# Optimization experiments

Hardware: AMD Instinct MI355X
Metric: run time of the kernel (lower is better)

The kernel has to match this reference:

```python
import jax, jax.numpy as jnp
import numpy as np

L, B, DW, DH, W, NG = 1024, 64, 300, 256, 2, 1
NEG = -1e25


def window_context(hx, w):
    """Concat of 2w+1 time-shifted copies of hx [L,B,D] -> [L,B,(2w+1)D].
    Order matches torch: shift-down by w..1, identity, shift-up by 1..w."""
    Lh = hx.shape[0]
    parts = []
    for i in range(w, -w - 1, -1):
        if i > 0:
            p = jnp.concatenate([jnp.zeros_like(hx[:i]), hx[:Lh - i]], axis=0)
        elif i < 0:
            k = -i
            p = jnp.concatenate([hx[k:], jnp.zeros_like(hx[:k])], axis=0)
        else:
            p = hx
        parts.append(p)
    return jnp.concatenate(parts, axis=2)


def setup_inputs() -> dict:
    key = jax.random.key(0)
    ks = jax.random.split(key, 11)
    E = (2 * W + 1) * DH
    std = 0.1  # reset_parameters('normal') uses N(0, 0.1)
    return {
        "src_seq": jax.random.normal(ks[0], (L, B, DW), jnp.float32),
        "h0": jax.random.normal(ks[1], (L + NG, B, DH), jnp.float32),
        "c0": jax.random.normal(ks[2], (L + NG, B, DH), jnp.float32),
        # word-gate params stacked over gates (i,l,r,f,s,o,u)
        "Ww": std * jax.random.normal(ks[3], (7, DH, E), jnp.float32),
        "Wu": std * jax.random.normal(ks[4], (7, DH, DW), jnp.float32),
        "Wv": std * jax.random.normal(ks[5], (7, DH, DH), jnp.float32),
        "Wb": std * jax.random.normal(ks[6], (7, DH), jnp.float32),
        # sentence-gate params stacked over gates (g,f,o)
        "Sw": std * jax.random.normal(ks[7], (3, DH, DH), jnp.float32),
        "Su": std * jax.random.normal(ks[8], (3, DH, DH), jnp.float32),
        "Sb": std * jax.random.normal(ks[9], (3, DH), jnp.float32),
        "src_len": jax.random.randint(ks[10], (B, 1), 1, L + 1, jnp.int32),
    }


def reference(src_seq, h0, c0, Ww, Wu, Wv, Wb, Sw, Su, Sb, src_len):
    # seq_mask[t, b] = True where t >= length[b]  -> [L, B, 1]
    seq_mask = (jnp.arange(L)[:, None] >= src_len[:, 0][None, :])[:, :, None]

    h_g1 = h0[L:]                                 # [1,B,DH] sentence node
    c_g1 = c0[L:]
    h_w1 = jnp.where(seq_mask, 0.0, h0[:L])       # [L,B,DH] word nodes
    c_w1 = jnp.where(seq_mask, 0.0, c0[:L])
    h_hat = h_w1.mean(axis=0)                     # [B,DH]
    hg = h_g1[0]                                  # [B,DH]

    # --- sentence node update (gate order g,f,o) ---
    fg = jax.nn.sigmoid(hg @ Sw[0].T + h_hat @ Su[0].T + Sb[0])[None]   # [1,B,DH]
    og = jax.nn.sigmoid(hg @ Sw[2].T + h_hat @ Su[2].T + Sb[2])[None]
    fi = jax.nn.sigmoid((hg @ Sw[1].T)[None]
                        + jnp.einsum('lbh,dh->lbd', h_w1, Su[1]) + Sb[1])
    fi = jnp.where(seq_mask, NEG, fi)
    fi_n = jax.nn.softmax(fi, axis=0)             # softmax over time
    c_g = fg * c_g1 + (fi_n * c_w1).sum(axis=0)
    h_g = og * jnp.tanh(c_g)

    # --- word node update (gate order i,l,r,f,s,o,u) ---
    eps = window_context(h_w1, W)                 # [L,B,(2W+1)DH]
    pre = (jnp.einsum('lbe,gde->glbd', eps, Ww)
           + jnp.einsum('lbw,gdw->glbd', src_seq, Wu)
           + jnp.einsum('bh,gdh->gbd', hg, Wv)[:, None]
           + Wb[:, None, None])                   # [7,L,B,DH]
    i_ = jax.nn.sigmoid(pre[0])
    l_ = jax.nn.sigmoid(pre[1])
    r_ = jax.nn.sigmoid(pre[2])
    f_ = jax.nn.sigmoid(pre[3])
    s_ = jax.nn.sigmoid(pre[4])
    o_ = jax.nn.sigmoid(pre[5])
    u_ = jnp.tanh(pre[6])

    gates = jnp.stack((l_, f_, r_, s_, i_), axis=0)          # [5,L,B,DH]
    gates = jnp.where(seq_mask[None], NEG, gates)
    gates_n = jax.nn.softmax(gates, axis=0)                  # softmax over 5 gates

    c_ctx = window_context(c_w1, 1)                          # window_size=1 (default)
    c_l, c_c, c_r = jnp.split(c_ctx, 3, axis=2)
    c_merged = jnp.stack(
        (c_l, c_c, c_r, jnp.broadcast_to(c_g1, c_c.shape), u_), axis=0)
    c_w = (gates_n * c_merged).sum(axis=0)
    c_w = jnp.where(seq_mask, 0.0, c_w)
    h_w = o_ * jnp.tanh(c_w)

    h_t = jnp.concatenate((h_w, h_g), axis=0)                # [L+1,B,DH]
    c_t = jnp.concatenate((c_w, c_g), axis=0)
    return (h_t, c_t)
```

## Files before the change

kernel.cpp:

```cpp
#include <hip/hip_runtime.h>
#include <hip/hip_bf16.h>

#define L_SEQ 1024
#define N_B   64
#define D_H   256
#define D_W   300
#define LDK   72
#define LDH   264

typedef __bf16 bf16x8 __attribute__((ext_vector_type(8)));
typedef float  f32x4  __attribute__((ext_vector_type(4)));
typedef unsigned short us8 __attribute__((ext_vector_type(8)));

#if defined(__has_builtin)
#if __has_builtin(__builtin_amdgcn_global_load_lds)
#define HAS_ASYNC_LDS 1
#endif
#endif

__device__ inline float b2f(unsigned short u){
    union { unsigned int i; float f; } v; v.i = ((unsigned int)u) << 16; return v.f;
}
__device__ inline unsigned short f2b(float f){
    union { float f; unsigned int i; } v; v.f = f;
    unsigned int u = v.i;
    return (unsigned short)((u + 0x7fffu + ((u >> 16) & 1u)) >> 16);
}
__device__ inline float sigf(float x){ return 1.0f / (1.0f + __expf(-x)); }
__device__ inline float tanhfast(float x){ return 1.0f - 2.0f / (__expf(2.0f*x) + 1.0f); }

__device__ inline float ldf(const void* p, size_t i, int isf){
    return isf ? ((const float*)p)[i] : b2f(((const unsigned short*)p)[i]);
}
__device__ inline unsigned short ld1b(const void* p, size_t i, int isf){
    return isf ? f2b(((const float*)p)[i]) : ((const unsigned short*)p)[i];
}
__device__ inline us8 ld8(const void* p, size_t i, int isf){
    if (isf){
        const float* f = (const float*)p + i;
        float4 x = *(const float4*)f;
        float4 y = *(const float4*)(f + 4);
        us8 r = { f2b(x.x), f2b(x.y), f2b(x.z), f2b(x.w),
                  f2b(y.x), f2b(y.y), f2b(y.z), f2b(y.w) };
        return r;
    }
    return *(const us8*)((const unsigned short*)p + i);
}
__device__ inline unsigned int ld2(const void* p, size_t i, int isf){
    if (isf){
        const float* f = (const float*)p + i;
        float2 x = *(const float2*)f;
        return (unsigned int)f2b(x.x) | ((unsigned int)f2b(x.y) << 16);
    }
    return *(const unsigned int*)((const unsigned short*)p + i);
}
__device__ inline float4 ldf4(const void* p, size_t i, int isf){
    if (isf) return *(const float4*)((const float*)p + i);
    unsigned long long v = *(const unsigned long long*)((const unsigned short*)p + i);
    float4 r;
    r.x = b2f((unsigned short)( v        & 0xffffu));
    r.y = b2f((unsigned short)((v >> 16) & 0xffffu));
    r.z = b2f((unsigned short)((v >> 32) & 0xffffu));
    r.w = b2f((unsigned short)( v >> 48));
    return r;
}

__device__ inline void stage16(const unsigned short* g, unsigned short* lds_base, int lane){
#ifdef HAS_ASYNC_LDS
    __builtin_amdgcn_global_load_lds(
        (const __attribute__((address_space(1))) unsigned int*)g,
        (__attribute__((address_space(3))) unsigned int*)lds_base, 16, 0, 0);
#else
    *(us8*)(lds_base + lane*8) = *(const us8*)g;
#endif
}

__global__ __launch_bounds__(256) void k_detect(const void* __restrict__ h0, int* __restrict__ flag)
{
    int tid = threadIdx.x;
    const unsigned short* u = (const unsigned short*)h0;
    int cnt = 0;
    #pragma unroll
    for (int i = 0; i < 4; i++){
        unsigned short v = u[(size_t)(tid * 4 + i) * 2];
        int e = (v >> 7) & 0xFF;
        cnt += (e >= 90 && e <= 150) ? 1 : 0;
    }
    __shared__ int red[256];
    red[tid] = cnt;
    __syncthreads();
    for (int s = 128; s > 0; s >>= 1){
        if (tid < s) red[tid] += red[tid + s];
        __syncthreads();
    }
    if (tid == 0) flag[0] = (red[0] > 512) ? 0 : 1;
}

__global__ __launch_bounds__(256) void k_conv_h(const void* __restrict__ h0,
    const int* __restrict__ slen, unsigned short* __restrict__ hpad, const int* __restrict__ flagp)
{
    int isf = flagp[0];
    int i = blockIdx.y;
    int idx = (blockIdx.x*256 + threadIdx.x)*8;
    int b = idx >> 8;
    int l = i - 2;
    us8 v = {0,0,0,0,0,0,0,0};
    if ((unsigned)l < 1024u && l < slen[b])
        v = ld8(h0, (size_t)l*16384 + idx, isf);
    *(us8*)(hpad + (size_t)i*16384 + idx) = v;
}

__global__ __launch_bounds__(256) void k_conv_src(const void* __restrict__ src,
    unsigned short* __restrict__ srcpad, const int* __restrict__ flagp)
{
    int isf = flagp[0];
    int gid = blockIdx.x*256 + threadIdx.x;
    int row = gid / 40, k = gid % 40, col = k*8;
    us8 v = {0,0,0,0,0,0,0,0};
    if (col + 8 <= 300) v = ld8(src, (size_t)row*300 + col, isf);
    else if (col < 300){
        for (int e = 0; e < 300 - col; ++e) v[e] = ld1b(src, (size_t)row*300 + col + e, isf);
    }
    *(us8*)(srcpad + (size_t)row*320 + col) = v;
}

__global__ __launch_bounds__(256) void k_conv_w(const void* __restrict__ Ww,
    const void* __restrict__ Wu, unsigned short* __restrict__ Wcat, const int* __restrict__ flagp)
{
    int isf = flagp[0];
    int gid = blockIdx.x*256 + threadIdx.x;
    int bx = gid / 22400, rem = gid % 22400;
    int h = rem / 448, rem2 = rem % 448;
    int rr = rem2 >> 2, c8 = rem2 & 3;
    int g = rr >> 4, d = bx*16 + (rr & 15);
    int k = h*32 + c8*8;
    size_t n = (size_t)g*256 + d;
    us8 v = {0,0,0,0,0,0,0,0};
    if (k < 1280) v = ld8(Ww, n*1280 + k, isf);
    else {
        int w = k - 1280;
        if (w + 8 <= 300) v = ld8(Wu, n*300 + w, isf);
        else if (w < 300){
            for (int e = 0; e < 300 - w; ++e) v[e] = ld1b(Wu, n*300 + w + e, isf);
        }
    }
    *(us8*)(Wcat + (size_t)gid*8) = v;
}

__global__ __launch_bounds__(256) void k_conv_su(const void* __restrict__ Su,
    unsigned short* __restrict__ Subf, const int* __restrict__ flagp)
{
    int isf = flagp[0];
    int gid = blockIdx.x*256 + threadIdx.x;
    *(us8*)(Subf + (size_t)gid*8) = ld8(Su, (size_t)65536 + (size_t)gid*8, isf);
}

__global__ __launch_bounds__(256) void k_hhat_fast(const unsigned short* __restrict__ hpad,
    float* __restrict__ hhat)
{
    int b = blockIdx.x, part = blockIdx.y, d = threadIdx.x;
    float s = 0.f;
    const unsigned short* p = hpad + (size_t)(2 + part*128)*16384 + b*256 + d;
    for (int ll = 0; ll < 128; ++ll)
        s += b2f(p[(size_t)ll*16384]);
    atomicAdd(&hhat[b*256 + d], s);
}

__global__ __launch_bounds__(1024) void k_hhat(const void* __restrict__ h0,
    const int* __restrict__ slen, float* __restrict__ hhat, const int* __restrict__ flagp)
{
    int isf = flagp[0];
    int b = blockIdx.x;
    int part = threadIdx.x >> 8;
    int d = threadIdx.x & 255;
    int lenb = slen[b];
    float s = 0.f;
    for (int l = part; l < lenb; l += 4)
        s += ldf(h0, (size_t)l*16384 + b*256 + d, isf);
    __shared__ float red[1024];
    red[threadIdx.x] = s;
    __syncthreads();
    if (part == 0)
        hhat[b*256 + d] = (red[d] + red[d+256] + red[d+512] + red[d+768]);
}

__global__ __launch_bounds__(256) void k_small(const void* __restrict__ h0,
    const float* __restrict__ hhat, const void* __restrict__ Sw,
    const void* __restrict__ Su, const void* __restrict__ Sb,
    float* __restrict__ fg, float* __restrict__ og, float* __restrict__ sg,
    const int* __restrict__ flagp, float hs)
{
    int isf = flagp[0];
    int b = blockIdx.x; int d = threadIdx.x;
    __shared__ float hgl[256], hhl[256];
    hgl[d] = ldf(h0, (size_t)16777216 + b*256 + d, isf);
    hhl[d] = hhat[b*256 + d] * hs;
    __syncthreads();
    size_t sw0 = (size_t)d*256, sw1 = (size_t)(256+d)*256, sw2 = (size_t)(512+d)*256;
    size_t su0 = (size_t)d*256, su2 = (size_t)(512+d)*256;
    float a0=0.f,a1=0.f,a2=0.f,a3=0.f,a4=0.f;
    #pragma unroll 4
    for (int h=0; h<256; h+=4){
        float4 w0 = ldf4(Sw, sw0+h, isf);
        float4 u0 = ldf4(Su, su0+h, isf);
        float4 w1 = ldf4(Sw, sw1+h, isf);
        float4 w2 = ldf4(Sw, sw2+h, isf);
        float4 u2 = ldf4(Su, su2+h, isf);
        float g0=hgl[h], g1=hgl[h+1], g2=hgl[h+2], g3=hgl[h+3];
        float q0=hhl[h], q1=hhl[h+1], q2=hhl[h+2], q3=hhl[h+3];
        a0 += g0*w0.x + g1*w0.y + g2*w0.z + g3*w0.w;
        a1 += q0*u0.x + q1*u0.y + q2*u0.z + q3*u0.w;
        a2 += g0*w1.x + g1*w1.y + g2*w1.z + g3*w1.w;
        a3 += g0*w2.x + g1*w2.y + g2*w2.z + g3*w2.w;
        a4 += q0*u2.x + q1*u2.y + q2*u2.z + q3*u2.w;
    }
    int i = b*256 + d;
    fg[i] = sigf(a0 + a1 + ldf(Sb, d, isf));
    sg[i] = a2 + ldf(Sb, 256 + d, isf);
    og[i] = sigf(a3 + a4 + ldf(Sb, 512 + d, isf));
}

__global__ __launch_bounds__(256) void k_hgwv(const void* __restrict__ h0,
    const void* __restrict__ Wv, const void* __restrict__ Wb,
    float* __restrict__ hgWvB, const int* __restrict__ flagp)
{
    int isf = flagp[0];
    int b = blockIdx.x, g = blockIdx.y, d = threadIdx.x;
    __shared__ float hgl[256];
    hgl[d] = ldf(h0, (size_t)16777216 + b*256 + d, isf);
    __syncthreads();
    size_t wv = ((size_t)g*256 + d)*256;
    float a = 0.f;
    #pragma unroll 4
    for (int h=0; h<256; h+=4){
        float4 w = ldf4(Wv, wv+h, isf);
        a += hgl[h]*w.x + hgl[h+1]*w.y + hgl[h+2]*w.z + hgl[h+3]*w.w;
    }
    hgWvB[(size_t)b*1792 + g*256 + d] = a + ldf(Wb, g*256 + d, isf);
}

__global__ __launch_bounds__(256) void k_fi_fast(const unsigned short* __restrict__ hpad,
    const void* __restrict__ c0, const unsigned short* __restrict__ Subf,
    const int* __restrict__ slen, const float* __restrict__ sg,
    float* __restrict__ numv, float* __restrict__ denv, const int* __restrict__ flagp)
{
    int isf = flagp[0];
    __shared__ unsigned short Hs[64*LDH];
    int tid = threadIdx.x;
    int b = blockIdx.x;
    int l0 = blockIdx.y * 64;
    int lenb = slen[b];
    #pragma unroll
    for (int i=0;i<8;i++){
        int c = tid + i*256;
        int r = c >> 5;
        int col = (c & 31) << 3;
        *(us8*)(Hs + r*LDH + col) =
            *(const us8*)(hpad + (size_t)(l0 + r + 2)*16384 + b*256 + col);
    }
    __syncthreads();
    int wv = tid >> 6, lane = tid & 63, qd = lane >> 4, lc = lane & 15;
    f32x4 zero4 = {0.f,0.f,0.f,0.f};
    for (int dci=0; dci<4; ++dci){
        int d = (wv*4 + dci) * 16 + lc;
        f32x4 acc[4];
        #pragma unroll
        for (int t=0;t<4;t++) acc[t] = zero4;
        #pragma unroll
        for (int ks=0; ks<8; ++ks){
            int k0 = ks*32 + qd*8;
            bf16x8 bb = *(const bf16x8*)(Subf + (size_t)d*256 + k0);
            #pragma unroll
            for (int lt=0; lt<4; ++lt){
                bf16x8 aa = *(const bf16x8*)(Hs + (lt*16 + lc)*LDH + k0);
                acc[lt] = __builtin_amdgcn_mfma_f32_16x16x32_bf16(aa, bb, acc[lt], 0, 0, 0);
            }
        }
        float sgv = sg[b*256 + d];
        float pn = 0.f, pd = 0.f;
        #pragma unroll
        for (int lt=0; lt<4; ++lt){
            #pragma unroll
            for (int r=0; r<4; ++r){
                int l = l0 + lt*16 + qd*4 + r;
                if (l < lenb){
                    float e = __expf(sigf(acc[lt][r] + sgv));
                    pd += e;
                    pn += e * ldf(c0, (size_t)l*16384 + b*256 + d, isf);
                }
            }
        }
        pn += __shfl_xor(pn, 16); pn += __shfl_xor(pn, 32);
        pd += __shfl_xor(pd, 16); pd += __shfl_xor(pd, 32);
        if (qd == 0){
            atomicAdd(&numv[b*256 + d], pn);
            atomicAdd(&denv[b*256 + d], pd);
        }
    }
}

__global__ __launch_bounds__(256) void k_fi(const void* __restrict__ h0,
    const void* __restrict__ c0, const void* __restrict__ Su,
    const int* __restrict__ slen, const float* __restrict__ sg,
    float* __restrict__ numv, float* __restrict__ denv, const int* __restrict__ flagp)
{
    int isf = flagp[0];
    __shared__ unsigned short Hs[64*LDH];
    int tid = threadIdx.x;
    int b = blockIdx.x;
    int l0 = blockIdx.y * 64;
    int lenb = slen[b];
    #pragma unroll
    for (int i=0;i<8;i++){
        int c = tid + i*256;
        int r = c >> 5;
        int col = (c & 31) << 3;
        int l = l0 + r;
        us8 v = {0,0,0,0,0,0,0,0};
        if (l < lenb)
            v = ld8(h0, (size_t)l*16384 + b*256 + col, isf);
        *(us8*)(Hs + r*LDH + col) = v;
    }
    __syncthreads();
    int wv = tid >> 6, lane = tid & 63, qd = lane >> 4, lc = lane & 15;
    f32x4 zero4 = {0.f,0.f,0.f,0.f};
    for (int dci=0; dci<4; ++dci){
        int d = (wv*4 + dci) * 16 + lc;
        f32x4 acc[4];
        #pragma unroll
        for (int t=0;t<4;t++) acc[t] = zero4;
        #pragma unroll
        for (int ks=0; ks<8; ++ks){
            int k0 = ks*32 + qd*8;
            union { us8 u; bf16x8 b; } cv; cv.u = ld8(Su, (size_t)65536 + (size_t)d*256 + k0, isf);
            bf16x8 bb = cv.b;
            #pragma unroll
            for (int lt=0; lt<4; ++lt){
                bf16x8 aa = *(const bf16x8*)(Hs + (lt*16 + lc)*LDH + k0);
                acc[lt] = __builtin_amdgcn_mfma_f32_16x16x32_bf16(aa, bb, acc[lt], 0, 0, 0);
            }
        }
        float sgv = sg[b*256 + d];
        float pn = 0.f, pd = 0.f;
        #pragma unroll
        for (int lt=0; lt<4; ++lt){
            #pragma unroll
            for (int r=0; r<4; ++r){
                int l = l0 + lt*16 + qd*4 + r;
                if (l < lenb){
                    float e = __expf(sigf(acc[lt][r] + sgv));
                    pd += e;
                    pn += e * ldf(c0, (size_t)l*16384 + b*256 + d, isf);
                }
            }
        }
        pn += __shfl_xor(pn, 16); pn += __shfl_xor(pn, 32);
        pd += __shfl_xor(pd, 16); pd += __shfl_xor(pd, 32);
        if (qd == 0){
            atomicAdd(&numv[b*256 + d], pn);
            atomicAdd(&denv[b*256 + d], pd);
        }
    }
}

__global__ __launch_bounds__(256) void k_cg(const void* __restrict__ c0,
    const float* __restrict__ fg, const float* __restrict__ og,
    const float* __restrict__ numv, const float* __restrict__ denv,
    float* __restrict__ outh, float* __restrict__ outc,
    const int* __restrict__ flagp)
{
    int isf = flagp[0];
    int i = blockIdx.x*256 + threadIdx.x;
    float cg1 = ldf(c0, (size_t)16777216 + i, isf);
    float cg = fg[i]*cg1 + numv[i]/denv[i];
    float hg = og[i]*tanhfast(cg);
    outh[(size_t)16777216 + i] = hg;
    outc[(size_t)16777216 + i] = cg;
}

__global__ __launch_bounds__(256, 2) void k_main_fast(
    const unsigned short* __restrict__ hpad, const unsigned short* __restrict__ srcpad,
    const unsigned short* __restrict__ Wcat, const void* __restrict__ c0,
    const int* __restrict__ slen, const float* __restrict__ hgWvB,
    float* __restrict__ outh, float* __restrict__ outc, const int* __restrict__ flagp)
{
    int isf = flagp[0];
    __shared__ unsigned short As[8192];
    __shared__ unsigned short Bs[3584];
    int tid = threadIdx.x;
    int d0 = blockIdx.x * 16;
    int m0 = blockIdx.y * 256;
    int wv = tid >> 6, lane = tid & 63, qd = lane >> 4, lc = lane & 15;

    int aoffH[4], aoffS[4];
    #pragma unroll
    for (int i=0;i<4;i++){
        int c = i*256 + tid;
        int r = c >> 2, sl = c & 3;
        int col = ((sl ^ ((r >> 1) & 3)) << 3);
        aoffH[i] = r*256 + col;
        aoffS[i] = r*320 + col;
    }
    int boff0s, boff1s;
    {
        int c = tid, r = c >> 2, sl = c & 3;
        boff0s = r*32 + ((sl ^ ((r >> 1) & 3)) << 3);
        c = 256 + tid; r = c >> 2; sl = c & 3;
        boff1s = r*32 + ((sl ^ ((r >> 1) & 3)) << 3);
    }
    const unsigned short* gB  = Wcat + (size_t)blockIdx.x * 50 * 3584;
    const unsigned short* gAh = hpad + (size_t)m0 * 256;
    const unsigned short* gAs = srcpad + (size_t)m0 * 320;

    int xch = (qd ^ ((lc >> 1) & 3)) << 3;
    int ra0 = (wv*64 +  0 + lc)*32 + xch;
    int ra1 = (wv*64 + 16 + lc)*32 + xch;
    int ra2 = (wv*64 + 32 + lc)*32 + xch;
    int ra3 = (wv*64 + 48 + lc)*32 + xch;
    int rb0 = ( 0 + lc)*32 + xch;
    int rb1 = (16 + lc)*32 + xch;
    int rb2 = (32 + lc)*32 + xch;
    int rb3 = (48 + lc)*32 + xch;
    int rb4 = (64 + lc)*32 + xch;
    int rb5 = (80 + lc)*32 + xch;
    int rb6 = (96 + lc)*32 + xch;

    f32x4 zero4 = {0.f,0.f,0.f,0.f};
    f32x4 acc[4][7];
    #pragma unroll
    for (int a=0;a<4;a++)
        #pragma unroll
        for (int g=0;g<7;g++) acc[a][g] = zero4;

    for (int h=0; h<50; ++h){
        __syncthreads();
        if (h < 40){
            const unsigned short* ga = gAh + (h>>3)*16384 + ((h&7)<<5);
            #pragma unroll
            for (int i=0;i<4;i++)
                stage16(ga + aoffH[i], As + i*2048 + wv*512, lane);
        } else {
            const unsigned short* ga = gAs + ((h-40)<<5);
            #pragma unroll
            for (int i=0;i<4;i++)
                stage16(ga + aoffS[i], As + i*2048 + wv*512, lane);
        }
        const unsigned short* gb = gB + h*3584;
        stage16(gb + boff0s, Bs + wv*512, lane);
        if (tid < 192)
            stage16(gb + boff1s, Bs + 2048 + wv*512, lane);
        __syncthreads();
        bf16x8 va0 = *(const bf16x8*)(As + ra0);
        bf16x8 va1 = *(const bf16x8*)(As + ra1);
        bf16x8 va2 = *(const bf16x8*)(As + ra2);
        bf16x8 va3 = *(const bf16x8*)(As + ra3);
        __builtin_amdgcn_s_setprio(1);
        {
            bf16x8 vb = *(const bf16x8*)(Bs + rb0);
            acc[0][0] = __builtin_amdgcn_mfma_f32_16x16x32_bf16(va0, vb, acc[0][0],0,0,0);
            acc[1][0] = __builtin_amdgcn_mfma_f32_16x16x32_bf16(va1, vb, acc[1][0],0,0,0);
            acc[2][0] = __builtin_amdgcn_mfma_f32_16x16x32_bf16(va2, vb, acc[2][0],0,0,0);
            acc[3][0] = __builtin_amdgcn_mfma_f32_16x16x32_bf16(va3, vb, acc[3][0],0,0,0);
        }
        {
            bf16x8 vb = *(const bf16x8*)(Bs + rb1);
            acc[0][1] = __builtin_amdgcn_mfma_f32_16x16x32_bf16(va0, vb, acc[0][1],0,0,0);
            acc[1][1] = __builtin_amdgcn_mfma_f32_16x16x32_bf16(va1, vb, acc[1][1],0,0,0);
            acc[2][1] = __builtin_amdgcn_mfma_f32_16x16x32_bf16(va2, vb, acc[2][1],0,0,0);
            acc[3][1] = __builtin_amdgcn_mfma_f32_16x16x32_bf16(va3, vb, acc[3][1],0,0,0);
        }
        {
            bf16x8 vb = *(const bf16x8*)(Bs + rb2);
            acc[0][2] = __builtin_amdgcn_mfma_f32_16x16x32_bf16(va0, vb, acc[0][2],0,0,0);
            acc[1][2] = __builtin_amdgcn_mfma_f32_16x16x32_bf16(va1, vb, acc[1][2],0,0,0);
            acc[2][2] = __builtin_amdgcn_mfma_f32_16x16x32_bf16(va2, vb, acc[2][2],0,0,0);
            acc[3][2] = __builtin_amdgcn_mfma_f32_16x16x32_bf16(va3, vb, acc[3][2],0,0,0);
        }
        {
            bf16x8 vb = *(const bf16x8*)(Bs + rb3);
            acc[0][3] = __builtin_amdgcn_mfma_f32_16x16x32_bf16(va0, vb, acc[0][3],0,0,0);
            acc[1][3] = __builtin_amdgcn_mfma_f32_16x16x32_bf16(va1, vb, acc[1][3],0,0,0);
            acc[2][3] = __builtin_amdgcn_mfma_f32_16x16x32_bf16(va2, vb, acc[2][3],0,0,0);
            acc[3][3] = __builtin_amdgcn_mfma_f32_16x16x32_bf16(va3, vb, acc[3][3],0,0,0);
        }
        {
            bf16x8 vb = *(const bf16x8*)(Bs + rb4);
            acc[0][4] = __builtin_amdgcn_mfma_f32_16x16x32_bf16(va0, vb, acc[0][4],0,0,0);
            acc[1][4] = __builtin_amdgcn_mfma_f32_16x16x32_bf16(va1, vb, acc[1][4],0,0,0);
            acc[2][4] = __builtin_amdgcn_mfma_f32_16x16x32_bf16(va2, vb, acc[2][4],0,0,0);
            acc[3][4] = __builtin_amdgcn_mfma_f32_16x16x32_bf16(va3, vb, acc[3][4],0,0,0);
        }
        {
            bf16x8 vb = *(const bf16x8*)(Bs + rb5);
            acc[0][5] = __builtin_amdgcn_mfma_f32_16x16x32_bf16(va0, vb, acc[0][5],0,0,0);
            acc[1][5] = __builtin_amdgcn_mfma_f32_16x16x32_bf16(va1, vb, acc[1][5],0,0,0);
            acc[2][5] = __builtin_amdgcn_mfma_f32_16x16x32_bf16(va2, vb, acc[2][5],0,0,0);
            acc[3][5] = __builtin_amdgcn_mfma_f32_16x16x32_bf16(va3, vb, acc[3][5],0,0,0);
        }
        {
            bf16x8 vb = *(const bf16x8*)(Bs + rb6);
            acc[0][6] = __builtin_amdgcn_mfma_f32_16x16x32_bf16(va0, vb, acc[0][6],0,0,0);
            acc[1][6] = __builtin_amdgcn_mfma_f32_16x16x32_bf16(va1, vb, acc[1][6],0,0,0);
            acc[2][6] = __builtin_amdgcn_mfma_f32_16x16x32_bf16(va2, vb, acc[2][6],0,0,0);
            acc[3][6] = __builtin_amdgcn_mfma_f32_16x16x32_bf16(va3, vb, acc[3][6],0,0,0);
        }
        __builtin_amdgcn_s_setprio(0);
    }

    int d = d0 + lc;
    #pragma unroll
    for (int mt=0; mt<4; ++mt){
        #pragma unroll
        for (int r=0; r<4; ++r){
            int m = m0 + wv*64 + mt*16 + qd*4 + r;
            int l = m >> 6, b = m & 63;
            size_t oi = (size_t)m*256 + d;
            int lenb = slen[b];
            float hw = 0.f, cw = 0.f;
            if (l < lenb){
                const float* hv = hgWvB + (size_t)b*1792 + d;
                float p0 = acc[mt][0][r] + hv[0];
                float p1 = acc[mt][1][r] + hv[256];
                float p2 = acc[mt][2][r] + hv[512];
                float p3 = acc[mt][3][r] + hv[768];
                float p4 = acc[mt][4][r] + hv[1024];
                float p5 = acc[mt][5][r] + hv[1280];
                float p6 = acc[mt][6][r] + hv[1536];
                float e_l = __expf(sigf(p1));
                float e_f = __expf(sigf(p3));
                float e_r = __expf(sigf(p2));
                float e_s = __expf(sigf(p4));
                float e_i = __expf(sigf(p0));
                float S = e_l + e_f + e_r + e_s + e_i;
                float u_ = tanhfast(p6);
                float cl = (l >= 1) ? ldf(c0, oi - 16384, isf) : 0.f;
                float cc = ldf(c0, oi, isf);
                float cr = (l + 1 < lenb) ? ldf(c0, oi + 16384, isf) : 0.f;
                float cg1 = ldf(c0, (size_t)16777216 + b*256 + d, isf);
                cw = (e_l*cl + e_f*cc + e_r*cr + e_s*cg1 + e_i*u_) / S;
                hw = sigf(p5) * tanhfast(cw);
            }
            outh[oi] = hw;
            outc[oi] = cw;
        }
    }
}

__global__ __launch_bounds__(256) void k_main(
    const void* __restrict__ src, const void* __restrict__ h0,
    const void* __restrict__ c0, const void* __restrict__ Ww,
    const void* __restrict__ Wu, const int* __restrict__ slen,
    const float* __restrict__ hgWvB,
    float* __restrict__ outh, float* __restrict__ outc,
    const int* __restrict__ flagp)
{
    int isf = flagp[0];
    __shared__ unsigned short As[128*LDK];
    __shared__ unsigned short Bs[112*LDK];
    int tid = threadIdx.x;
    int m0 = blockIdx.x * 128;
    int d0 = blockIdx.y * 16;
    int wv = tid >> 6, lane = tid & 63, qd = lane >> 4, lc = lane & 15;

    int ar[4], acol[4], al[4], ab[4], alen[4];
    #pragma unroll
    for (int i=0;i<4;i++){
        int c = tid + i*256;
        ar[i] = c >> 3; acol[i] = (c & 7) << 3;
        int m = m0 + ar[i];
        al[i] = m >> 6; ab[i] = m & 63;
        alen[i] = slen[ab[i]];
    }

    f32x4 zero4 = {0.f,0.f,0.f,0.f};
    f32x4 acc[2][7];
    #pragma unroll
    for (int a=0;a<2;a++)
        #pragma unroll
        for (int g=0;g<7;g++) acc[a][g] = zero4;

    for (int kt=0; kt<25; ++kt){
        __syncthreads();
        if (kt < 20){
            int j = kt >> 2;
            int koff = (kt & 3) << 6;
            #pragma unroll
            for (int i=0;i<4;i++){
                int lp = al[i] + j - 2;
                us8 v = {0,0,0,0,0,0,0,0};
                if ((unsigned)lp < 1024u && lp < alen[i])
                    v = ld8(h0, (size_t)lp*16384 + ab[i]*256 + koff + acol[i], isf);
                *(us8*)(As + ar[i]*LDK + acol[i]) = v;
            }
            #pragma unroll
            for (int i=0;i<4;i++){
                int c = tid + i*256;
                if (c < 896){
                    int rr = c >> 3, col = (c & 7) << 3;
                    int g = rr >> 4, d = d0 + (rr & 15);
                    *(us8*)(Bs + rr*LDK + col) =
                        ld8(Ww, ((size_t)g*256 + d)*1280 + j*256 + koff + col, isf);
                }
            }
        } else {
            int w0 = (kt - 20) << 6;
            #pragma unroll
            for (int i=0;i<16;i++){
                int c = tid + i*256;
                int r = c >> 5, wi = (c & 31) << 1;
                int w = w0 + wi;
                int m = m0 + r;
                unsigned int v = 0;
                if (w < 300) v = ld2(src, (size_t)m*300 + w, isf);
                *(unsigned int*)(As + r*LDK + wi) = v;
            }
            #pragma unroll
            for (int i=0;i<14;i++){
                int c = tid + i*256;
                int rr = c >> 5, wi = (c & 31) << 1;
                int w = w0 + wi;
                int g = rr >> 4, d = d0 + (rr & 15);
                unsigned int v = 0;
                if (w < 300) v = ld2(Wu, ((size_t)g*256 + d)*300 + w, isf);
                *(unsigned int*)(Bs + rr*LDK + wi) = v;
            }
        }
        __syncthreads();
        #pragma unroll
        for (int ks=0; ks<2; ++ks){
            int k0 = (ks << 5) + (qd << 3);
            bf16x8 a0 = *(const bf16x8*)(As + (wv*32 + lc)*LDK + k0);
            bf16x8 a1 = *(const bf16x8*)(As + (wv*32 + 16 + lc)*LDK + k0);
            #pragma unroll
            for (int g=0; g<7; ++g){
                bf16x8 bg = *(const bf16x8*)(Bs + (g*16 + lc)*LDK + k0);
                acc[0][g] = __builtin_amdgcn_mfma_f32_16x16x32_bf16(a0, bg, acc[0][g], 0,0,0);
                acc[1][g] = __builtin_amdgcn_mfma_f32_16x16x32_bf16(a1, bg, acc[1][g], 0,0,0);
            }
        }
    }

    int d = d0 + lc;
    #pragma unroll
    for (int mt=0; mt<2; ++mt){
        #pragma unroll
        for (int r=0; r<4; ++r){
            int m = m0 + wv*32 + mt*16 + qd*4 + r;
            int l = m >> 6, b = m & 63;
            size_t oi = (size_t)m*256 + d;
            int lenb = slen[b];
            float hw = 0.f, cw = 0.f;
            if (l < lenb){
                const float* hv = hgWvB + (size_t)b*1792 + d;
                float p0 = acc[mt][0][r] + hv[0];
                float p1 = acc[mt][1][r] + hv[256];
                float p2 = acc[mt][2][r] + hv[512];
                float p3 = acc[mt][3][r] + hv[768];
                float p4 = acc[mt][4][r] + hv[1024];
                float p5 = acc[mt][5][r] + hv[1280];
                float p6 = acc[mt][6][r] + hv[1536];
                float e_l = __expf(sigf(p1));
                float e_f = __expf(sigf(p3));
                float e_r = __expf(sigf(p2));
                float e_s = __expf(sigf(p4));
                float e_i = __expf(sigf(p0));
                float S = e_l + e_f + e_r + e_s + e_i;
                float u_ = tanhfast(p6);
                float cl = (l >= 1) ? ldf(c0, oi - 16384, isf) : 0.f;
                float cc = ldf(c0, oi, isf);
                float cr = (l + 1 < lenb) ? ldf(c0, oi + 16384, isf) : 0.f;
                float cg1 = ldf(c0, (size_t)16777216 + b*256 + d, isf);
                cw = (e_l*cl + e_f*cc + e_r*cr + e_s*cg1 + e_i*u_) / S;
                hw = sigf(p5) * tanhfast(cw);
            }
            outh[oi] = hw;
            outc[oi] = cw;
        }
    }
}

extern "C" void kernel_launch(void* const* d_in, const int* in_sizes, int n_in,
                              void* d_out, int out_size, void* d_ws, size_t ws_size,
                              hipStream_t stream)
{
    const void* src = d_in[0];
    const void* h0  = d_in[1];
    const void* c0  = d_in[2];
    const void* Ww  = d_in[3];
    const void* Wu  = d_in[4];
    const void* Wv  = d_in[5];
    const void* Wb  = d_in[6];
    const void* Sw  = d_in[7];
    const void* Su  = d_in[8];
    const void* Sb  = d_in[9];
    const int* slen = (const int*)d_in[10];

    float* outh = (float*)d_out;
    float* outc = outh + (size_t)1025*64*256;

    float* ws    = (float*)d_ws;
    float* numv  = ws;
    float* denv  = ws + 16384;
    float* hhat  = ws + 32768;
    float* fg    = ws + 49152;
    float* og    = ws + 65536;
    float* sg    = ws + 81920;
    float* hgWvB = ws + 98304;
    int*   flag  = (int*)(ws + 212992);

    unsigned short* bfbase = (unsigned short*)(ws + 213024);
    unsigned short* hpad   = bfbase;
    unsigned short* srcpad = bfbase + (size_t)16842752;
    unsigned short* Wcat   = bfbase + (size_t)37814272;
    unsigned short* Subf   = bfbase + (size_t)40681472;
    const size_t NEED = 852096 + (size_t)40747008*2;

    hipLaunchKernelGGL(k_detect, dim3(1), dim3(256), 0, stream, h0, flag);
    hipMemsetAsync(ws, 0, (size_t)3*16384*sizeof(float), stream);

    if (ws_size >= NEED){
        hipLaunchKernelGGL(k_conv_h,  dim3(8,1028), dim3(256), 0, stream, h0, slen, hpad, flag);
        hipLaunchKernelGGL(k_conv_src, dim3(10240), dim3(256), 0, stream, src, srcpad, flag);
        hipLaunchKernelGGL(k_conv_w,   dim3(1400),  dim3(256), 0, stream, Ww, Wu, Wcat, flag);
        hipLaunchKernelGGL(k_conv_su,  dim3(32),    dim3(256), 0, stream, Su, Subf, flag);
        hipLaunchKernelGGL(k_hhat_fast, dim3(64,8), dim3(256), 0, stream, hpad, hhat);
        hipLaunchKernelGGL(k_small, dim3(64), dim3(256), 0, stream, h0, hhat, Sw, Su, Sb,
                           fg, og, sg, flag, 1.0f/1024.0f);
        hipLaunchKernelGGL(k_hgwv, dim3(64,7), dim3(256), 0, stream, h0, Wv, Wb, hgWvB, flag);
        hipLaunchKernelGGL(k_fi_fast, dim3(64,16), dim3(256), 0, stream, hpad, c0, Subf, slen,
                           sg, numv, denv, flag);
        hipLaunchKernelGGL(k_cg, dim3(64), dim3(256), 0, stream, c0, fg, og, numv, denv,
                           outh, outc, flag);
        hipLaunchKernelGGL(k_main_fast, dim3(16,256), dim3(256), 0, stream,
                           hpad, srcpad, Wcat, c0, slen, hgWvB, outh, outc, flag);
    } else {
        hipLaunchKernelGGL(k_hhat, dim3(64), dim3(1024), 0, stream, h0, slen, hhat, flag);
        hipLaunchKernelGGL(k_small, dim3(64), dim3(256), 0, stream, h0, hhat, Sw, Su, Sb,
                           fg, og, sg, flag, 1.0f/1024.0f);
        hipLaunchKernelGGL(k_hgwv, dim3(64,7), dim3(256), 0, stream, h0, Wv, Wb, hgWvB, flag);
        hipLaunchKernelGGL(k_fi, dim3(64,16), dim3(256), 0, stream, h0, c0, Su, slen,
                           sg, numv, denv, flag);
        hipLaunchKernelGGL(k_cg, dim3(64), dim3(256), 0, stream, c0, fg, og, numv, denv,
                           outh, outc, flag);
        hipLaunchKernelGGL(k_main, dim3(512,16), dim3(256), 0, stream,
                           src, h0, c0, Ww, Wu, slen, hgWvB, outh, outc, flag);
    }
}
```

Measured before the change: 854.9 us.

## Stage two K-panels per barrier pair and swizzle block order in main GEMM

```diff
diff --git a/kernel.cpp b/kernel.cpp
--- a/kernel.cpp
+++ b/kernel.cpp
@@ -385,11 +385,14 @@
     float* __restrict__ outh, float* __restrict__ outc, const int* __restrict__ flagp)
 {
     int isf = flagp[0];
-    __shared__ unsigned short As[8192];
-    __shared__ unsigned short Bs[3584];
+    __shared__ unsigned short As[2][8192];
+    __shared__ unsigned short Bs[2][3584];
     int tid = threadIdx.x;
-    int d0 = blockIdx.x * 16;
-    int m0 = blockIdx.y * 256;
+    int hlin = blockIdx.x;
+    int bx = (hlin >> 3) & 15;
+    int by = ((hlin & 7) << 5) + (hlin >> 7);
+    int d0 = bx * 16;
+    int m0 = by * 256;
     int wv = tid >> 6, lane = tid & 63, qd = lane >> 4, lc = lane & 15;
 
     int aoffH[4], aoffS[4];
@@ -408,7 +411,7 @@
         c = 256 + tid; r = c >> 2; sl = c & 3;
         boff1s = r*32 + ((sl ^ ((r >> 1) & 3)) << 3);
     }
-    const unsigned short* gB  = Wcat + (size_t)blockIdx.x * 50 * 3584;
+    const unsigned short* gB  = Wcat + (size_t)bx * 50 * 3584;
     const unsigned short* gAh = hpad + (size_t)m0 * 256;
     const unsigned short* gAs = srcpad + (size_t)m0 * 320;
 
@@ -432,80 +435,82 @@
         #pragma unroll
         for (int g=0;g<7;g++) acc[a][g] = zero4;
 
-    for (int h=0; h<50; ++h){
+#define STAGE_SUB(pan_, p_) do {                                                 \
+        int pp_ = (p_);                                                          \
+        unsigned short* asb_ = &As[pan_][0];                                     \
+        unsigned short* bsb_ = &Bs[pan_][0];                                     \
+        if (pp_ < 40){                                                           \
+            const unsigned short* ga_ = gAh + (pp_>>3)*16384 + ((pp_&7)<<5);     \
+            _Pragma("unroll")                                                    \
+            for (int i_=0;i_<4;i_++)                                             \
+                stage16(ga_ + aoffH[i_], asb_ + i_*2048 + wv*512, lane);         \
+        } else {                                                                 \
+            const unsigned short* ga_ = gAs + ((pp_-40)<<5);                     \
+            _Pragma("unroll")                                                    \
+            for (int i_=0;i_<4;i_++)                                             \
+                stage16(ga_ + aoffS[i_], asb_ + i_*2048 + wv*512, lane);         \
+        }                                                                        \
+        const unsigned short* gb_ = gB + pp_*3584;                               \
+        stage16(gb_ + boff0s, bsb_ + wv*512, lane);                              \
+        if (tid < 192) stage16(gb_ + boff1s, bsb_ + 2048 + wv*512, lane);        \
+    } while(0)
+
+#define COMP_SUB(pan_) do {                                                      \
+        const unsigned short* as_ = &As[pan_][0];                                \
+        const unsigned short* bs_ = &Bs[pan_][0];                                \
+        bf16x8 va0 = *(const bf16x8*)(as_ + ra0);                                \
+        bf16x8 va1 = *(const bf16x8*)(as_ + ra1);                                \
+        bf16x8 va2 = *(const bf16x8*)(as_ + ra2);                                \
+        bf16x8 va3 = *(const bf16x8*)(as_ + ra3);                                \
+        bf16x8 vb0 = *(const bf16x8*)(bs_ + rb0);                                \
+        bf16x8 vb1 = *(const bf16x8*)(bs_ + rb1);                                \
+        bf16x8 vb2 = *(const bf16x8*)(bs_ + rb2);                                \
+        bf16x8 vb3 = *(const bf16x8*)(bs_ + rb3);                                \
+        bf16x8 vb4 = *(const bf16x8*)(bs_ + rb4);                                \
+        bf16x8 vb5 = *(const bf16x8*)(bs_ + rb5);                                \
+        bf16x8 vb6 = *(const bf16x8*)(bs_ + rb6);                                \
+        __builtin_amdgcn_s_setprio(1);                                           \
+        acc[0][0] = __builtin_amdgcn_mfma_f32_16x16x32_bf16(va0, vb0, acc[0][0],0,0,0); \
+        acc[1][0] = __builtin_amdgcn_mfma_f32_16x16x32_bf16(va1, vb0, acc[1][0],0,0,0); \
+        acc[2][0] = __builtin_amdgcn_mfma_f32_16x16x32_bf16(va2, vb0, acc[2][0],0,0,0); \
+        acc[3][0] = __builtin_amdgcn_mfma_f32_16x16x32_bf16(va3, vb0, acc[3][0],0,0,0); \
+        acc[0][1] = __builtin_amdgcn_mfma_f32_16x16x32_bf16(va0, vb1, acc[0][1],0,0,0); \
+        acc[1][1] = __builtin_amdgcn_mfma_f32_16x16x32_bf16(va1, vb1, acc[1][1],0,0,0); \
+        acc[2][1] = __builtin_amdgcn_mfma_f32_16x16x32_bf16(va2, vb1, acc[2][1],0,0,0); \
+        acc[3][1] = __builtin_amdgcn_mfma_f32_16x16x32_bf16(va3, vb1, acc[3][1],0,0,0); \
+        acc[0][2] = __builtin_amdgcn_mfma_f32_16x16x32_bf16(va0, vb2, acc[0][2],0,0,0); \
+        acc[1][2] = __builtin_amdgcn_mfma_f32_16x16x32_bf16(va1, vb2, acc[1][2],0,0,0); \
+        acc[2][2] = __builtin_amdgcn_mfma_f32_16x16x32_bf16(va2, vb2, acc[2][2],0,0,0); \
+        acc[3][2] = __builtin_amdgcn_mfma_f32_16x16x32_bf16(va3, vb2, acc[3][2],0,0,0); \
+        acc[0][3] = __builtin_amdgcn_mfma_f32_16x16x32_bf16(va0, vb3, acc[0][3],0,0,0); \
+        acc[1][3] = __builtin_amdgcn_mfma_f32_16x16x32_bf16(va1, vb3, acc[1][3],0,0,0); \
+        acc[2][3] = __builtin_amdgcn_mfma_f32_16x16x32_bf16(va2, vb3, acc[2][3],0,0,0); \
+        acc[3][3] = __builtin_amdgcn_mfma_f32_16x16x32_bf16(va3, vb3, acc[3][3],0,0,0); \
+        acc[0][4] = __builtin_amdgcn_mfma_f32_16x16x32_bf16(va0, vb4, acc[0][4],0,0,0); \
+        acc[1][4] = __builtin_amdgcn_mfma_f32_16x16x32_bf16(va1, vb4, acc[1][4],0,0,0); \
+        acc[2][4] = __builtin_amdgcn_mfma_f32_16x16x32_bf16(va2, vb4, acc[2][4],0,0,0); \
+        acc[3][4] = __builtin_amdgcn_mfma_f32_16x16x32_bf16(va3, vb4, acc[3][4],0,0,0); \
+        acc[0][5] = __builtin_amdgcn_mfma_f32_16x16x32_bf16(va0, vb5, acc[0][5],0,0,0); \
+        acc[1][5] = __builtin_amdgcn_mfma_f32_16x16x32_bf16(va1, vb5, acc[1][5],0,0,0); \
+        acc[2][5] = __builtin_amdgcn_mfma_f32_16x16x32_bf16(va2, vb5, acc[2][5],0,0,0); \
+        acc[3][5] = __builtin_amdgcn_mfma_f32_16x16x32_bf16(va3, vb5, acc[3][5],0,0,0); \
+        acc[0][6] = __builtin_amdgcn_mfma_f32_16x16x32_bf16(va0, vb6, acc[0][6],0,0,0); \
+        acc[1][6] = __builtin_amdgcn_mfma_f32_16x16x32_bf16(va1, vb6, acc[1][6],0,0,0); \
+        acc[2][6] = __builtin_amdgcn_mfma_f32_16x16x32_bf16(va2, vb6, acc[2][6],0,0,0); \
+        acc[3][6] = __builtin_amdgcn_mfma_f32_16x16x32_bf16(va3, vb6, acc[3][6],0,0,0); \
+        __builtin_amdgcn_s_setprio(0);                                           \
+    } while(0)
+
+    for (int h=0; h<25; ++h){
         __syncthreads();
-        if (h < 40){
-            const unsigned short* ga = gAh + (h>>3)*16384 + ((h&7)<<5);
-            #pragma unroll
-            for (int i=0;i<4;i++)
-                stage16(ga + aoffH[i], As + i*2048 + wv*512, lane);
-        } else {
-            const unsigned short* ga = gAs + ((h-40)<<5);
-            #pragma unroll
-            for (int i=0;i<4;i++)
-                stage16(ga + aoffS[i], As + i*2048 + wv*512, lane);
-        }
-        const unsigned short* gb = gB + h*3584;
-        stage16(gb + boff0s, Bs + wv*512, lane);
-        if (tid < 192)
-            stage16(gb + boff1s, Bs + 2048 + wv*512, lane);
+        STAGE_SUB(0, 2*h);
+        STAGE_SUB(1, 2*h + 1);
         __syncthreads();
-        bf16x8 va0 = *(const bf16x8*)(As + ra0);
-        bf16x8 va1 = *(const bf16x8*)(As + ra1);
-        bf16x8 va2 = *(const bf16x8*)(As + ra2);
-        bf16x8 va3 = *(const bf16x8*)(As + ra3);
-        __builtin_amdgcn_s_setprio(1);
-        {
-            bf16x8 vb = *(const bf16x8*)(Bs + rb0);
-            acc[0][0] = __builtin_amdgcn_mfma_f32_16x16x32_bf16(va0, vb, acc[0][0],0,0,0);
-            acc[1][0] = __builtin_amdgcn_mfma_f32_16x16x32_bf16(va1, vb, acc[1][0],0,0,0);
-            acc[2][0] = __builtin_amdgcn_mfma_f32_16x16x32_bf16(va2, vb, acc[2][0],0,0,0);
-            acc[3][0] = __builtin_amdgcn_mfma_f32_16x16x32_bf16(va3, vb, acc[3][0],0,0,0);
-        }
-        {
-            bf16x8 vb = *(const bf16x8*)(Bs + rb1);
-            acc[0][1] = __builtin_amdgcn_mfma_f32_16x16x32_bf16(va0, vb, acc[0][1],0,0,0);
-            acc[1][1] = __builtin_amdgcn_mfma_f32_16x16x32_bf16(va1, vb, acc[1][1],0,0,0);
-            acc[2][1] = __builtin_amdgcn_mfma_f32_16x16x32_bf16(va2, vb, acc[2][1],0,0,0);
-            acc[3][1] = __builtin_amdgcn_mfma_f32_16x16x32_bf16(va3, vb, acc[3][1],0,0,0);
-        }
-        {
-            bf16x8 vb = *(const bf16x8*)(Bs + rb2);
-            acc[0][2] = __builtin_amdgcn_mfma_f32_16x16x32_bf16(va0, vb, acc[0][2],0,0,0);
-            acc[1][2] = __builtin_amdgcn_mfma_f32_16x16x32_bf16(va1, vb, acc[1][2],0,0,0);
-            acc[2][2] = __builtin_amdgcn_mfma_f32_16x16x32_bf16(va2, vb, acc[2][2],0,0,0);
-            acc[3][2] = __builtin_amdgcn_mfma_f32_16x16x32_bf16(va3, vb, acc[3][2],0,0,0);
-        }
-        {
-            bf16x8 vb = *(const bf16x8*)(Bs + rb3);
-            acc[0][3] = __builtin_amdgcn_mfma_f32_16x16x32_bf16(va0, vb, acc[0][3],0,0,0);
-            acc[1][3] = __builtin_amdgcn_mfma_f32_16x16x32_bf16(va1, vb, acc[1][3],0,0,0);
-            acc[2][3] = __builtin_amdgcn_mfma_f32_16x16x32_bf16(va2, vb, acc[2][3],0,0,0);
-            acc[3][3] = __builtin_amdgcn_mfma_f32_16x16x32_bf16(va3, vb, acc[3][3],0,0,0);
-        }
-        {
-            bf16x8 vb = *(const bf16x8*)(Bs + rb4);
-            acc[0][4] = __builtin_amdgcn_mfma_f32_16x16x32_bf16(va0, vb, acc[0][4],0,0,0);
-            acc[1][4] = __builtin_amdgcn_mfma_f32_16x16x32_bf16(va1, vb, acc[1][4],0,0,0);
-            acc[2][4] = __builtin_amdgcn_mfma_f32_16x16x32_bf16(va2, vb, acc[2][4],0,0,0);
-            acc[3][4] = __builtin_amdgcn_mfma_f32_16x16x32_bf16(va3, vb, acc[3][4],0,0,0);
-        }
-        {
-            bf16x8 vb = *(const bf16x8*)(Bs + rb5);
-            acc[0][5] = __builtin_amdgcn_mfma_f32_16x16x32_bf16(va0, vb, acc[0][5],0,0,0);
-            acc[1][5] = __builtin_amdgcn_mfma_f32_16x16x32_bf16(va1, vb, acc[1][5],0,0,0);
-            acc[2][5] = __builtin_amdgcn_mfma_f32_16x16x32_bf16(va2, vb, acc[2][5],0,0,0);
-            acc[3][5] = __builtin_amdgcn_mfma_f32_16x16x32_bf16(va3, vb, acc[3][5],0,0,0);
-        }
-        {
-            bf16x8 vb = *(const bf16x8*)(Bs + rb6);
-            acc[0][6] = __builtin_amdgcn_mfma_f32_16x16x32_bf16(va0, vb, acc[0][6],0,0,0);
-            acc[1][6] = __builtin_amdgcn_mfma_f32_16x16x32_bf16(va1, vb, acc[1][6],0,0,0);
-            acc[2][6] = __builtin_amdgcn_mfma_f32_16x16x32_bf16(va2, vb, acc[2][6],0,0,0);
-            acc[3][6] = __builtin_amdgcn_mfma_f32_16x16x32_bf16(va3, vb, acc[3][6],0,0,0);
-        }
-        __builtin_amdgcn_s_setprio(0);
-    }
+        COMP_SUB(0);
+        COMP_SUB(1);
+    }
+#undef STAGE_SUB
+#undef COMP_SUB
 
     int d = d0 + lc;
     #pragma unroll
@@ -731,7 +736,7 @@
                            sg, numv, denv, flag);
         hipLaunchKernelGGL(k_cg, dim3(64), dim3(256), 0, stream, c0, fg, og, numv, denv,
                            outh, outc, flag);
-        hipLaunchKernelGGL(k_main_fast, dim3(16,256), dim3(256), 0, stream,
+        hipLaunchKernelGGL(k_main_fast, dim3(4096), dim3(256), 0, stream,
                            hpad, srcpad, Wcat, c0, slen, hgWvB, outh, outc, flag);
     } else {
         hipLaunchKernelGGL(k_hhat, dim3(64), dim3(1024), 0, stream, h0, slen, hhat, flag);
```

Measured after the change: 891.8 us. 1.04x slower.
